# Kernel optimization log

Measured on AMD Instinct MI355X. Metric: run time of the kernel, lower is better.

The kernel has to match this reference:

```python
import jax, jax.numpy as jnp
import numpy as np

N_NODES = 100000
N_EDGES = 3200000
N_GRAPHS = 2048
MOL_DIM = 78
HID = 32
OUT = 128
N_LAYERS = 5
BN_EPS = 1e-5


def setup_inputs() -> dict:
    key = jax.random.key(0)
    ks = jax.random.split(key, 16)
    x = jax.random.normal(ks[0], (N_NODES, MOL_DIM), dtype=jnp.float32)
    edge_index = jax.random.randint(ks[1], (2, N_EDGES), 0, N_NODES, dtype=jnp.int32)
    batch = jnp.sort(jax.random.randint(ks[2], (N_NODES,), 0, N_GRAPHS, dtype=jnp.int32))
    def lin(k, fan_in, shape):
        b = 1.0 / np.sqrt(fan_in)
        return jax.random.uniform(k, shape, jnp.float32, -b, b)
    # layer 0 MLP (78 -> 32 -> 32)
    w1_0 = lin(ks[3], MOL_DIM, (MOL_DIM, HID))
    b1_0 = lin(ks[4], MOL_DIM, (HID,))
    w2_0 = lin(ks[5], HID, (HID, HID))
    b2_0 = lin(ks[6], HID, (HID,))
    # layers 1..4 MLPs (32 -> 32 -> 32), stacked
    w1 = lin(ks[7], HID, (N_LAYERS - 1, HID, HID))
    b1 = lin(ks[8], HID, (N_LAYERS - 1, HID))
    w2 = lin(ks[9], HID, (N_LAYERS - 1, HID, HID))
    b2 = lin(ks[10], HID, (N_LAYERS - 1, HID))
    # BatchNorm affine params per layer
    gamma = jnp.ones((N_LAYERS, HID), jnp.float32)
    beta = jnp.zeros((N_LAYERS, HID), jnp.float32)
    # final fc (32 -> 128)
    fc_w = lin(ks[11], HID, (HID, OUT))
    fc_b = lin(ks[12], HID, (OUT,))
    return {"x": x, "edge_index": edge_index, "batch": batch,
            "w1_0": w1_0, "b1_0": b1_0, "w2_0": w2_0, "b2_0": b2_0,
            "w1": w1, "b1": b1, "w2": w2, "b2": b2,
            "gamma": gamma, "beta": beta, "fc_w": fc_w, "fc_b": fc_b}


def _gin_layer(x, src, dst, W1, B1, W2, B2, g, bt):
    # GIN aggregation: (1+eps)*x + sum_{j in N(i)} x_j, eps = 0
    agg = x + jax.ops.segment_sum(x[src], dst, num_segments=N_NODES)
    h = jnp.maximum(agg @ W1 + B1, 0.0)   # Linear + ReLU
    h = h @ W2 + B2                        # Linear
    h = jnp.maximum(h, 0.0)                # outer act before BN
    mean = jnp.mean(h, axis=0)
    var = jnp.mean(jnp.square(h - mean), axis=0)  # biased (training BN)
    return (h - mean) * jax.lax.rsqrt(var + BN_EPS) * g + bt


def reference(x, edge_index, batch, w1_0, b1_0, w2_0, b2_0,
              w1, b1, w2, b2, gamma, beta, fc_w, fc_b):
    src, dst = edge_index[0], edge_index[1]
    h = _gin_layer(x, src, dst, w1_0, b1_0, w2_0, b2_0, gamma[0], beta[0])
    for i in range(N_LAYERS - 1):
        h = _gin_layer(h, src, dst, w1[i], b1[i], w2[i], b2[i],
                       gamma[i + 1], beta[i + 1])
    pooled = jax.ops.segment_sum(h, batch, num_segments=N_GRAPHS)  # [G, HID]
    out = jnp.maximum(pooled @ fc_w + fc_b, 0.0)  # dropout is identity in eval
    return out
```

## Files before the change

kernel.cpp:

```cpp
#include <hip/hip_runtime.h>
#include <hip/hip_fp16.h>

#define N_NODES 100000
#define N_EDGES 3200000
#define N_GRAPHS 2048
#define MOL 78
#define HID 32
#define OUTD 128
#define BN_EPS 1e-5f

#define NBUCK ((N_NODES + 255) / 256)
#define BCAP2 9216
#define EPB 4096
#define P1_BLOCKS ((N_EDGES + EPB - 1) / EPB)

#define NPH 4
#define CPL_BLOCKS (N_NODES / (8 * NPH))

#define NCOPY 64

__device__ inline unsigned int pkh2(float a, float b) {
    __half2 h = __halves2half2(__float2half_rn(a), __float2half_rn(b));
    return *(unsigned int*)&h;
}
__device__ inline float hlo(unsigned int v) {
    __half2 h = *(__half2*)&v;
    return __low2float(h);
}
__device__ inline float hhi(unsigned int v) {
    __half2 h = *(__half2*)&v;
    return __high2float(h);
}


__global__ __launch_bounds__(256) void part1_kernel(const int* __restrict__ src,
                                                    const int* __restrict__ dst,
                                                    int* __restrict__ gcur,
                                                    int* __restrict__ staging) {
    __shared__ int hist[NBUCK];
    __shared__ int lofs[NBUCK];
    __shared__ int lcur[NBUCK];
    __shared__ int gb[NBUCK];
    __shared__ int pk[EPB];
    __shared__ unsigned short bkt[EPB];
    __shared__ int sc[256];
    const int t = threadIdx.x;
    const int base = blockIdx.x * EPB;
    const int nedge = min(EPB, N_EDGES - base);

    for (int i = t; i < NBUCK; i += 256) hist[i] = 0;
    __syncthreads();
    for (int i = t; i < nedge; i += 256) atomicAdd(&hist[dst[base + i] >> 8], 1);
    __syncthreads();

    int a0 = (2 * t < NBUCK) ? hist[2 * t] : 0;
    int a1 = (2 * t + 1 < NBUCK) ? hist[2 * t + 1] : 0;
    int tot = a0 + a1;
    sc[t] = tot;
    __syncthreads();
    for (int off = 1; off < 256; off <<= 1) {
        int add = (t >= off) ? sc[t - off] : 0;
        __syncthreads();
        sc[t] += add;
        __syncthreads();
    }
    int excl = sc[t] - tot;
    if (2 * t < NBUCK) { lofs[2 * t] = excl; lcur[2 * t] = excl; }
    if (2 * t + 1 < NBUCK) { lofs[2 * t + 1] = excl + a0; lcur[2 * t + 1] = excl + a0; }
    __syncthreads();

    for (int i = t; i < nedge; i += 256) {
        int d = dst[base + i];
        int s = src[base + i];
        int b = d >> 8;
        int p = atomicAdd(&lcur[b], 1);
        pk[p] = (s << 8) | (d & 255);
        bkt[p] = (unsigned short)b;
    }
    __syncthreads();

    for (int b = t; b < NBUCK; b += 256) {
        int c = lcur[b] - lofs[b];
        gb[b] = c ? atomicAdd(&gcur[b], c) : 0;
    }
    __syncthreads();

    for (int i = t; i < nedge; i += 256) {
        int b = bkt[i];
        staging[(size_t)b * BCAP2 + gb[b] + (i - lofs[b])] = pk[i];
    }
}

__global__ void csrbase_kernel(const int* __restrict__ gcur, int* __restrict__ bbase,
                               int* __restrict__ row_start) {
    int t = threadIdx.x;
    int a0 = (2 * t < NBUCK) ? gcur[2 * t] : 0;
    int a1 = (2 * t + 1 < NBUCK) ? gcur[2 * t + 1] : 0;
    int tot = a0 + a1;
    __shared__ int sc[256];
    sc[t] = tot;
    __syncthreads();
    for (int off = 1; off < 256; off <<= 1) {
        int add = (t >= off) ? sc[t - off] : 0;
        __syncthreads();
        sc[t] += add;
        __syncthreads();
    }
    int excl = sc[t] - tot;
    if (2 * t < NBUCK) bbase[2 * t] = excl;
    if (2 * t + 1 < NBUCK) bbase[2 * t + 1] = excl + a0;
    if (t == 0) row_start[N_NODES] = N_EDGES;
}

__global__ __launch_bounds__(256) void part2_kernel(const int* __restrict__ gcur,
                                                    const int* __restrict__ bbase,
                                                    const int* __restrict__ staging,
                                                    int* __restrict__ row_start,
                                                    int* __restrict__ csr,
                                                    float* __restrict__ degf) {
    int b = blockIdx.x, t = threadIdx.x;
    __shared__ int ldeg[256];
    __shared__ int lex[256];
    __shared__ int sc[256];
    ldeg[t] = 0;
    __syncthreads();
    int cnt = gcur[b];
    int base = bbase[b];
    const int* sp = staging + (size_t)b * BCAP2;
    for (int i = t; i < cnt; i += 256) atomicAdd(&ldeg[sp[i] & 255], 1);
    __syncthreads();
    int v = ldeg[t];
    sc[t] = v;
    __syncthreads();
    for (int off = 1; off < 256; off <<= 1) {
        int add = (t >= off) ? sc[t - off] : 0;
        __syncthreads();
        sc[t] += add;
        __syncthreads();
    }
    int excl = sc[t] - v;
    int node = b * 256 + t;
    if (node < N_NODES) {
        row_start[node] = base + excl;
        degf[node] = 1.0f + (float)v;
    }
    lex[t] = base + excl;
    __syncthreads();
    for (int i = t; i < cnt; i += 256) {
        int pk = sp[i];
        int p = atomicAdd(&lex[pk & 255], 1);
        csr[p] = pk >> 8;
    }
}


__global__ void gcnt_kernel(const int* __restrict__ batch, int* __restrict__ cnt) {
    int g = blockIdx.x * blockDim.x + threadIdx.x;
    if (g >= N_GRAPHS) return;
    auto lb = [&](int key) {
        int lo = 0, hi = N_NODES;
        while (lo < hi) {
            int mid = (lo + hi) >> 1;
            if (batch[mid] < key) lo = mid + 1; else hi = mid;
        }
        return lo;
    };
    cnt[g] = lb(g + 1) - lb(g);
}


__global__ __launch_bounds__(256) void proj78_kernel(const float* __restrict__ in,
                                                     const float* __restrict__ W1,
                                                     unsigned int* __restrict__ y) {
    __shared__ float w1s[MOL * HID];
    for (int i = threadIdx.x; i < MOL * HID; i += 256) w1s[i] = W1[i];
    __syncthreads();
    const int node = blockIdx.x * 256 + threadIdx.x;
    if (node >= N_NODES) return;
    const float* row = in + (size_t)node * MOL;
    float acc[HID];
#pragma unroll
    for (int j = 0; j < HID; j++) acc[j] = 0.f;
    const float4* w1v = (const float4*)w1s;
    for (int k = 0; k < MOL; k++) {
        float xv = row[k];
#pragma unroll
        for (int q = 0; q < 8; q++) {
            float4 wv = w1v[k * 8 + q];
            acc[4 * q + 0] = fmaf(xv, wv.x, acc[4 * q + 0]);
            acc[4 * q + 1] = fmaf(xv, wv.y, acc[4 * q + 1]);
            acc[4 * q + 2] = fmaf(xv, wv.z, acc[4 * q + 2]);
            acc[4 * q + 3] = fmaf(xv, wv.w, acc[4 * q + 3]);
        }
    }
    uint4* o = (uint4*)(y + (size_t)node * 16);
#pragma unroll
    for (int g = 0; g < 4; g++) {
        uint4 u;
        u.x = pkh2(acc[8 * g + 0], acc[8 * g + 1]);
        u.y = pkh2(acc[8 * g + 2], acc[8 * g + 3]);
        u.z = pkh2(acc[8 * g + 4], acc[8 * g + 5]);
        u.w = pkh2(acc[8 * g + 6], acc[8 * g + 7]);
        o[g] = u;
    }
}


template <int MODE>
__global__ __launch_bounds__(256) void gma_kernel(
    const unsigned int* __restrict__ y, const int* __restrict__ rs, const int* __restrict__ csr,
    const float* __restrict__ degf, const float* __restrict__ scsh_prev,
    const float* __restrict__ B1, const float* __restrict__ W1, const float* __restrict__ W2,
    const float* __restrict__ B2, __half* __restrict__ out, float* __restrict__ sums,
    const int* __restrict__ batch, float* __restrict__ pooledraw) {
    __shared__ float ldsu[8][NPH][HID];
    __shared__ float ldsv[8][NPH][HID];
    __shared__ float w2T[HID][HID + 1];
    __shared__ float w1T[HID][HID + 1];
    __shared__ float ssum[64];
    const int t = threadIdx.x;
    const int hw = t >> 5;
    const int hl = t & 31;
    const int s = hl >> 2;
    const int q = hl & 3;
    const int c = hl;

    for (int idx = t; idx < HID * HID; idx += 256) {
        int k = idx >> 5, cc = idx & 31;
        w2T[cc][k] = W2[idx];
        if (MODE != 0) w1T[cc][k] = W1[idx];
    }
    if (t < 64) ssum[t] = 0.f;
    __syncthreads();

    float4 p0a, p0b, p1a, p1b;
    if (MODE == 0) {
        p0a = ((const float4*)B1)[2 * q];
        p0b = ((const float4*)B1)[2 * q + 1];
    } else {
        p0a = ((const float4*)scsh_prev)[2 * q];
        p0b = ((const float4*)scsh_prev)[2 * q + 1];
        p1a = ((const float4*)(scsh_prev + HID))[2 * q];
        p1b = ((const float4*)(scsh_prev + HID))[2 * q + 1];
    }

    const int n0 = (blockIdx.x * 8 + hw) * NPH;
    const uint4* rows = (const uint4*)y;

    for (int u = 0; u < NPH; u++) {
        const int n = n0 + u;
        float acc[8];
#pragma unroll
        for (int i = 0; i < 8; i++) acc[i] = 0.f;
        if (s == 0) {
            uint4 w = rows[(size_t)n * 4 + q];
            acc[0] = hlo(w.x); acc[1] = hhi(w.x);
            acc[2] = hlo(w.y); acc[3] = hhi(w.y);
            acc[4] = hlo(w.z); acc[5] = hhi(w.z);
            acc[6] = hlo(w.w); acc[7] = hhi(w.w);
        }
        int e0 = rs[n], e1 = rs[n + 1];
        int k = e0 + s;
        for (; k + 8 < e1; k += 16) {
            uint4 a = rows[(size_t)csr[k] * 4 + q];
            uint4 b = rows[(size_t)csr[k + 8] * 4 + q];
            acc[0] += hlo(a.x) + hlo(b.x);
            acc[1] += hhi(a.x) + hhi(b.x);
            acc[2] += hlo(a.y) + hlo(b.y);
            acc[3] += hhi(a.y) + hhi(b.y);
            acc[4] += hlo(a.z) + hlo(b.z);
            acc[5] += hhi(a.z) + hhi(b.z);
            acc[6] += hlo(a.w) + hlo(b.w);
            acc[7] += hhi(a.w) + hhi(b.w);
        }
        if (k < e1) {
            uint4 a = rows[(size_t)csr[k] * 4 + q];
            acc[0] += hlo(a.x); acc[1] += hhi(a.x);
            acc[2] += hlo(a.y); acc[3] += hhi(a.y);
            acc[4] += hlo(a.z); acc[5] += hhi(a.z);
            acc[6] += hlo(a.w); acc[7] += hhi(a.w);
        }
#pragma unroll
        for (int m = 4; m <= 16; m <<= 1) {
#pragma unroll
            for (int i = 0; i < 8; i++) acc[i] += __shfl_xor(acc[i], m, 32);
        }
        if (s == 0) {
            float o[8];
            if (MODE == 0) {
                o[0] = fmaxf(acc[0] + p0a.x, 0.f); o[1] = fmaxf(acc[1] + p0a.y, 0.f);
                o[2] = fmaxf(acc[2] + p0a.z, 0.f); o[3] = fmaxf(acc[3] + p0a.w, 0.f);
                o[4] = fmaxf(acc[4] + p0b.x, 0.f); o[5] = fmaxf(acc[5] + p0b.y, 0.f);
                o[6] = fmaxf(acc[6] + p0b.z, 0.f); o[7] = fmaxf(acc[7] + p0b.w, 0.f);
            } else {
                float dn = degf[n];
                o[0] = fmaf(acc[0], p0a.x, dn * p1a.x);
                o[1] = fmaf(acc[1], p0a.y, dn * p1a.y);
                o[2] = fmaf(acc[2], p0a.z, dn * p1a.z);
                o[3] = fmaf(acc[3], p0a.w, dn * p1a.w);
                o[4] = fmaf(acc[4], p0b.x, dn * p1b.x);
                o[5] = fmaf(acc[5], p0b.y, dn * p1b.y);
                o[6] = fmaf(acc[6], p0b.z, dn * p1b.z);
                o[7] = fmaf(acc[7], p0b.w, dn * p1b.w);
            }
            float4* d = (float4*)&ldsu[hw][u][q * 8];
            d[0] = make_float4(o[0], o[1], o[2], o[3]);
            d[1] = make_float4(o[4], o[5], o[6], o[7]);
        }
    }

    const float b2c = B2[c];
    float sl = 0.f, sq = 0.f;

    if (MODE == 0) {
        float h[NPH];
#pragma unroll
        for (int u = 0; u < NPH; u++) h[u] = b2c;
#pragma unroll
        for (int qq = 0; qq < 8; qq++) {
            float wa = w2T[c][4 * qq + 0], wb = w2T[c][4 * qq + 1];
            float wc2 = w2T[c][4 * qq + 2], wd = w2T[c][4 * qq + 3];
#pragma unroll
            for (int u = 0; u < NPH; u++) {
                float4 vv = ((const float4*)&ldsu[hw][u][0])[qq];
                h[u] = fmaf(vv.x, wa, h[u]);
                h[u] = fmaf(vv.y, wb, h[u]);
                h[u] = fmaf(vv.z, wc2, h[u]);
                h[u] = fmaf(vv.w, wd, h[u]);
            }
        }
#pragma unroll
        for (int u = 0; u < NPH; u++) {
            float hv = fmaxf(h[u], 0.f);
            out[(size_t)(n0 + u) * 32 + c] = __float2half_rn(hv);
            sl += hv;
            sq += hv * hv;
        }
    } else {
        const float b1c = B1[c];
        float tv[NPH];
#pragma unroll
        for (int u = 0; u < NPH; u++) tv[u] = b1c;
#pragma unroll
        for (int qq = 0; qq < 8; qq++) {
            float wa = w1T[c][4 * qq + 0], wb = w1T[c][4 * qq + 1];
            float wc1 = w1T[c][4 * qq + 2], wd = w1T[c][4 * qq + 3];
#pragma unroll
            for (int u = 0; u < NPH; u++) {
                float4 uu = ((const float4*)&ldsu[hw][u][0])[qq];
                tv[u] = fmaf(uu.x, wa, tv[u]);
                tv[u] = fmaf(uu.y, wb, tv[u]);
                tv[u] = fmaf(uu.z, wc1, tv[u]);
                tv[u] = fmaf(uu.w, wd, tv[u]);
            }
        }
#pragma unroll
        for (int u = 0; u < NPH; u++) ldsv[hw][u][c] = fmaxf(tv[u], 0.f);
        float h[NPH];
#pragma unroll
        for (int u = 0; u < NPH; u++) h[u] = b2c;
#pragma unroll
        for (int qq = 0; qq < 8; qq++) {
            float wa = w2T[c][4 * qq + 0], wb = w2T[c][4 * qq + 1];
            float wc2 = w2T[c][4 * qq + 2], wd = w2T[c][4 * qq + 3];
#pragma unroll
            for (int u = 0; u < NPH; u++) {
                float4 vv = ((const float4*)&ldsv[hw][u][0])[qq];
                h[u] = fmaf(vv.x, wa, h[u]);
                h[u] = fmaf(vv.y, wb, h[u]);
                h[u] = fmaf(vv.z, wc2, h[u]);
                h[u] = fmaf(vv.w, wd, h[u]);
            }
        }
#pragma unroll
        for (int u = 0; u < NPH; u++) {
            float hv = fmaxf(h[u], 0.f);
            if (MODE == 2) {
                atomicAdd(&pooledraw[batch[n0 + u] * HID + c], hv);
            } else {
                out[(size_t)(n0 + u) * 32 + c] = __float2half_rn(hv);
            }
            sl += hv;
            sq += hv * hv;
        }
    }

    atomicAdd(&ssum[c], sl);
    atomicAdd(&ssum[32 + c], sq);
    __syncthreads();
    if (t < 64) atomicAdd(&sums[(blockIdx.x & (NCOPY - 1)) * 64 + t], ssum[t]);
}


__global__ void bnfin_kernel(const float* __restrict__ sums, const float* __restrict__ g,
                             const float* __restrict__ bt, float* __restrict__ scsh) {
    __shared__ float red[64];
    int t = threadIdx.x;
    if (t < 64) {
        float acc = 0.f;
#pragma unroll 8
        for (int k = 0; k < NCOPY; k++) acc += sums[k * 64 + t];
        red[t] = acc;
    }
    __syncthreads();
    if (t < HID) {
        float m = red[t] * (1.0f / N_NODES);
        float var = red[HID + t] * (1.0f / N_NODES) - m * m;
        var = fmaxf(var, 0.f);
        float sc = g[t] * rsqrtf(var + BN_EPS);
        scsh[t] = sc;
        scsh[HID + t] = bt[t] - m * sc;
    }
}


__global__ void fc_kernel(const float* __restrict__ praw, const int* __restrict__ cnt,
                          const float* __restrict__ scsh4, const float* __restrict__ fcw,
                          const float* __restrict__ fcb, float* __restrict__ out) {
    __shared__ float w[HID * OUTD];
    __shared__ float aff[2 * HID];
    for (int i = threadIdx.x; i < HID * OUTD; i += 256) w[i] = fcw[i];
    if (threadIdx.x < 2 * HID) aff[threadIdx.x] = scsh4[threadIdx.x];
    __syncthreads();
    int idx = blockIdx.x * 256 + threadIdx.x;
    if (idx >= N_GRAPHS * OUTD) return;
    int g = idx >> 7;
    int o = idx & 127;
    float cg = (float)cnt[g];
    float acc = fcb[o];
#pragma unroll
    for (int k = 0; k < HID; k++) {
        float paff = fmaf(praw[g * HID + k], aff[k], cg * aff[HID + k]);
        acc = fmaf(paff, w[k * OUTD + o], acc);
    }
    out[idx] = fmaxf(acc, 0.f);
}


extern "C" void kernel_launch(void* const* d_in, const int* in_sizes, int n_in,
                              void* d_out, int out_size, void* d_ws, size_t ws_size,
                              hipStream_t stream) {
    const float* x = (const float*)d_in[0];
    const int* ei = (const int*)d_in[1];
    const int* batch = (const int*)d_in[2];
    const float* w1_0 = (const float*)d_in[3];
    const float* b1_0 = (const float*)d_in[4];
    const float* w2_0 = (const float*)d_in[5];
    const float* b2_0 = (const float*)d_in[6];
    const float* w1 = (const float*)d_in[7];
    const float* b1 = (const float*)d_in[8];
    const float* w2 = (const float*)d_in[9];
    const float* b2 = (const float*)d_in[10];
    const float* gamma = (const float*)d_in[11];
    const float* beta = (const float*)d_in[12];
    const float* fc_w = (const float*)d_in[13];
    const float* fc_b = (const float*)d_in[14];
    float* out = (float*)d_out;

    const int* e_src = ei;
    const int* e_dst = ei + N_EDGES;

    char* ws = (char*)d_ws;
    size_t off = 0;
    auto alloc = [&](size_t n) {
        void* p = ws + off;
        off += (n + 255) & ~(size_t)255;
        return p;
    };
    int* row_start = (int*)alloc((size_t)(N_NODES + 1) * 4);
    int* csr = (int*)alloc((size_t)N_EDGES * 4);
    int* bbase = (int*)alloc((size_t)NBUCK * 4);
    int* staging = (int*)alloc((size_t)NBUCK * BCAP2 * 4);
    unsigned int* hA = (unsigned int*)alloc((size_t)N_NODES * 16 * 4);
    unsigned int* hB = (unsigned int*)alloc((size_t)N_NODES * 16 * 4);
    float* degf = (float*)alloc((size_t)N_NODES * 4);
    float* scsh = (float*)alloc(5 * 2 * HID * 4);
    int* cnt = (int*)alloc((size_t)N_GRAPHS * 4);
    size_t zero_base = off;
    int* gcur = (int*)alloc((size_t)NBUCK * 4);
    float* bnsums = (float*)alloc((size_t)5 * NCOPY * 64 * 4);
    float* pooled = (float*)alloc((size_t)N_GRAPHS * HID * 4);
    size_t zero_len = off - zero_base;

    hipMemsetAsync(ws + zero_base, 0, zero_len, stream);

    part1_kernel<<<P1_BLOCKS, 256, 0, stream>>>(e_src, e_dst, gcur, staging);
    csrbase_kernel<<<1, 256, 0, stream>>>(gcur, bbase, row_start);
    part2_kernel<<<NBUCK, 256, 0, stream>>>(gcur, bbase, staging, row_start, csr, degf);
    gcnt_kernel<<<(N_GRAPHS + 255) / 256, 256, 0, stream>>>(batch, cnt);

    const int nodeBlocks = (N_NODES + 255) / 256;

    proj78_kernel<<<nodeBlocks, 256, 0, stream>>>(x, w1_0, hA);
    gma_kernel<0><<<CPL_BLOCKS, 256, 0, stream>>>(
        hA, row_start, csr, nullptr, nullptr, b1_0, nullptr, w2_0, b2_0, (__half*)hB, bnsums,
        nullptr, nullptr);
    bnfin_kernel<<<1, 64, 0, stream>>>(bnsums, gamma, beta, scsh);

    unsigned int* cur = hB;
    unsigned int* nxt = hA;
    for (int l = 1; l < 5; l++) {
        int i = l - 1;
        if (l < 4) {
            gma_kernel<1><<<CPL_BLOCKS, 256, 0, stream>>>(
                cur, row_start, csr, degf, scsh + (l - 1) * 2 * HID, b1 + (size_t)i * HID,
                w1 + (size_t)i * HID * HID, w2 + (size_t)i * HID * HID, b2 + (size_t)i * HID,
                (__half*)nxt, bnsums + (size_t)l * NCOPY * 64, nullptr, nullptr);
            unsigned int* tmp = cur; cur = nxt; nxt = tmp;
        } else {
            gma_kernel<2><<<CPL_BLOCKS, 256, 0, stream>>>(
                cur, row_start, csr, degf, scsh + (l - 1) * 2 * HID, b1 + (size_t)i * HID,
                w1 + (size_t)i * HID * HID, w2 + (size_t)i * HID * HID, b2 + (size_t)i * HID,
                nullptr, bnsums + (size_t)l * NCOPY * 64, batch, pooled);
        }
        bnfin_kernel<<<1, 64, 0, stream>>>(bnsums + (size_t)l * NCOPY * 64, gamma + l * HID,
                                           beta + l * HID, scsh + l * 2 * HID);
    }

    fc_kernel<<<(N_GRAPHS * OUTD + 255) / 256, 256, 0, stream>>>(
        pooled, cnt, scsh + 4 * 2 * HID, fc_w, fc_b, out);
}
```

Before: 410.9 us.

## Split fused gather-MLP kernel into separate aggregation and MLP kernels

The fused gather+MLP kernel is split in two. A standalone aggregation kernel assigns one node per 32-lane group and writes fp32 neighbor sums to a new buffer, and a separate MLP kernel reads those sums to apply BN scale/shift, the two linear layers and the statistics. The aim is more parallelism and latency hiding in the gather, which previously walked 4 nodes serially per half-wave. The cost is an extra fp32 round trip through global memory (12.8 MB written and read per layer) and five more kernel launches.

```diff
diff --git a/kernel.cpp b/kernel.cpp
--- a/kernel.cpp
+++ b/kernel.cpp
@@ -206,13 +206,68 @@
 }
 
 
+__global__ __launch_bounds__(256) void agg_kernel(const unsigned int* __restrict__ y,
+                                                  const int* __restrict__ rs,
+                                                  const int* __restrict__ csr,
+                                                  float* __restrict__ agg) {
+    int gt = blockIdx.x * blockDim.x + threadIdx.x;
+    int node = gt >> 5;
+    if (node >= N_NODES) return;
+    int hl = threadIdx.x & 31;
+    int s = hl >> 2;
+    int q = hl & 3;
+    const uint4* rows = (const uint4*)y;
+    float acc[8];
+#pragma unroll
+    for (int i = 0; i < 8; i++) acc[i] = 0.f;
+    if (s == 0) {
+        uint4 u = rows[(size_t)node * 4 + q];
+        acc[0] = hlo(u.x); acc[1] = hhi(u.x);
+        acc[2] = hlo(u.y); acc[3] = hhi(u.y);
+        acc[4] = hlo(u.z); acc[5] = hhi(u.z);
+        acc[6] = hlo(u.w); acc[7] = hhi(u.w);
+    }
+    int e0 = rs[node], e1 = rs[node + 1];
+    int k = e0 + s;
+    for (; k + 8 < e1; k += 16) {
+        uint4 a = rows[(size_t)csr[k] * 4 + q];
+        uint4 b = rows[(size_t)csr[k + 8] * 4 + q];
+        acc[0] += hlo(a.x) + hlo(b.x);
+        acc[1] += hhi(a.x) + hhi(b.x);
+        acc[2] += hlo(a.y) + hlo(b.y);
+        acc[3] += hhi(a.y) + hhi(b.y);
+        acc[4] += hlo(a.z) + hlo(b.z);
+        acc[5] += hhi(a.z) + hhi(b.z);
+        acc[6] += hlo(a.w) + hlo(b.w);
+        acc[7] += hhi(a.w) + hhi(b.w);
+    }
+    if (k < e1) {
+        uint4 a = rows[(size_t)csr[k] * 4 + q];
+        acc[0] += hlo(a.x); acc[1] += hhi(a.x);
+        acc[2] += hlo(a.y); acc[3] += hhi(a.y);
+        acc[4] += hlo(a.z); acc[5] += hhi(a.z);
+        acc[6] += hlo(a.w); acc[7] += hhi(a.w);
+    }
+#pragma unroll
+    for (int m = 4; m <= 16; m <<= 1) {
+#pragma unroll
+        for (int i = 0; i < 8; i++) acc[i] += __shfl_xor(acc[i], m, 32);
+    }
+    if (s == 0) {
+        float4* o = (float4*)(agg + (size_t)node * HID + q * 8);
+        o[0] = make_float4(acc[0], acc[1], acc[2], acc[3]);
+        o[1] = make_float4(acc[4], acc[5], acc[6], acc[7]);
+    }
+}
+
+
 template <int MODE>
-__global__ __launch_bounds__(256) void gma_kernel(
-    const unsigned int* __restrict__ y, const int* __restrict__ rs, const int* __restrict__ csr,
-    const float* __restrict__ degf, const float* __restrict__ scsh_prev,
-    const float* __restrict__ B1, const float* __restrict__ W1, const float* __restrict__ W2,
-    const float* __restrict__ B2, __half* __restrict__ out, float* __restrict__ sums,
-    const int* __restrict__ batch, float* __restrict__ pooledraw) {
+__global__ __launch_bounds__(256) void mlp_kernel(
+    const float* __restrict__ aggb, const float* __restrict__ degf,
+    const float* __restrict__ scsh_prev, const float* __restrict__ B1,
+    const float* __restrict__ W1, const float* __restrict__ W2, const float* __restrict__ B2,
+    __half* __restrict__ out, float* __restrict__ sums, const int* __restrict__ batch,
+    float* __restrict__ pooledraw) {
     __shared__ float ldsu[8][NPH][HID];
     __shared__ float ldsv[8][NPH][HID];
     __shared__ float w2T[HID][HID + 1];
@@ -220,10 +275,7 @@
     __shared__ float ssum[64];
     const int t = threadIdx.x;
     const int hw = t >> 5;
-    const int hl = t & 31;
-    const int s = hl >> 2;
-    const int q = hl & 3;
-    const int c = hl;
+    const int c = t & 31;
 
     for (int idx = t; idx < HID * HID; idx += 256) {
         int k = idx >> 5, cc = idx & 31;
@@ -233,86 +285,15 @@
     if (t < 64) ssum[t] = 0.f;
     __syncthreads();
 
-    float4 p0a, p0b, p1a, p1b;
-    if (MODE == 0) {
-        p0a = ((const float4*)B1)[2 * q];
-        p0b = ((const float4*)B1)[2 * q + 1];
-    } else {
-        p0a = ((const float4*)scsh_prev)[2 * q];
-        p0b = ((const float4*)scsh_prev)[2 * q + 1];
-        p1a = ((const float4*)(scsh_prev + HID))[2 * q];
-        p1b = ((const float4*)(scsh_prev + HID))[2 * q + 1];
-    }
-
     const int n0 = (blockIdx.x * 8 + hw) * NPH;
-    const uint4* rows = (const uint4*)y;
-
-    for (int u = 0; u < NPH; u++) {
-        const int n = n0 + u;
-        float acc[8];
-#pragma unroll
-        for (int i = 0; i < 8; i++) acc[i] = 0.f;
-        if (s == 0) {
-            uint4 w = rows[(size_t)n * 4 + q];
-            acc[0] = hlo(w.x); acc[1] = hhi(w.x);
-            acc[2] = hlo(w.y); acc[3] = hhi(w.y);
-            acc[4] = hlo(w.z); acc[5] = hhi(w.z);
-            acc[6] = hlo(w.w); acc[7] = hhi(w.w);
-        }
-        int e0 = rs[n], e1 = rs[n + 1];
-        int k = e0 + s;
-        for (; k + 8 < e1; k += 16) {
-            uint4 a = rows[(size_t)csr[k] * 4 + q];
-            uint4 b = rows[(size_t)csr[k + 8] * 4 + q];
-            acc[0] += hlo(a.x) + hlo(b.x);
-            acc[1] += hhi(a.x) + hhi(b.x);
-            acc[2] += hlo(a.y) + hlo(b.y);
-            acc[3] += hhi(a.y) + hhi(b.y);
-            acc[4] += hlo(a.z) + hlo(b.z);
-            acc[5] += hhi(a.z) + hhi(b.z);
-            acc[6] += hlo(a.w) + hlo(b.w);
-            acc[7] += hhi(a.w) + hhi(b.w);
-        }
-        if (k < e1) {
-            uint4 a = rows[(size_t)csr[k] * 4 + q];
-            acc[0] += hlo(a.x); acc[1] += hhi(a.x);
-            acc[2] += hlo(a.y); acc[3] += hhi(a.y);
-            acc[4] += hlo(a.z); acc[5] += hhi(a.z);
-            acc[6] += hlo(a.w); acc[7] += hhi(a.w);
-        }
-#pragma unroll
-        for (int m = 4; m <= 16; m <<= 1) {
-#pragma unroll
-            for (int i = 0; i < 8; i++) acc[i] += __shfl_xor(acc[i], m, 32);
-        }
-        if (s == 0) {
-            float o[8];
-            if (MODE == 0) {
-                o[0] = fmaxf(acc[0] + p0a.x, 0.f); o[1] = fmaxf(acc[1] + p0a.y, 0.f);
-                o[2] = fmaxf(acc[2] + p0a.z, 0.f); o[3] = fmaxf(acc[3] + p0a.w, 0.f);
-                o[4] = fmaxf(acc[4] + p0b.x, 0.f); o[5] = fmaxf(acc[5] + p0b.y, 0.f);
-                o[6] = fmaxf(acc[6] + p0b.z, 0.f); o[7] = fmaxf(acc[7] + p0b.w, 0.f);
-            } else {
-                float dn = degf[n];
-                o[0] = fmaf(acc[0], p0a.x, dn * p1a.x);
-                o[1] = fmaf(acc[1], p0a.y, dn * p1a.y);
-                o[2] = fmaf(acc[2], p0a.z, dn * p1a.z);
-                o[3] = fmaf(acc[3], p0a.w, dn * p1a.w);
-                o[4] = fmaf(acc[4], p0b.x, dn * p1b.x);
-                o[5] = fmaf(acc[5], p0b.y, dn * p1b.y);
-                o[6] = fmaf(acc[6], p0b.z, dn * p1b.z);
-                o[7] = fmaf(acc[7], p0b.w, dn * p1b.w);
-            }
-            float4* d = (float4*)&ldsu[hw][u][q * 8];
-            d[0] = make_float4(o[0], o[1], o[2], o[3]);
-            d[1] = make_float4(o[4], o[5], o[6], o[7]);
-        }
-    }
-
     const float b2c = B2[c];
     float sl = 0.f, sq = 0.f;
 
     if (MODE == 0) {
+        const float b1c = B1[c];
+#pragma unroll
+        for (int u = 0; u < NPH; u++)
+            ldsu[hw][u][c] = fmaxf(aggb[(size_t)(n0 + u) * HID + c] + b1c, 0.f);
         float h[NPH];
 #pragma unroll
         for (int u = 0; u < NPH; u++) h[u] = b2c;
@@ -337,7 +318,13 @@
             sq += hv * hv;
         }
     } else {
+        const float scv = scsh_prev[c], shv = scsh_prev[HID + c];
         const float b1c = B1[c];
+#pragma unroll
+        for (int u = 0; u < NPH; u++) {
+            int n = n0 + u;
+            ldsu[hw][u][c] = fmaf(aggb[(size_t)n * HID + c], scv, degf[n] * shv);
+        }
         float tv[NPH];
 #pragma unroll
         for (int u = 0; u < NPH; u++) tv[u] = b1c;
@@ -473,6 +460,7 @@
     int* staging = (int*)alloc((size_t)NBUCK * BCAP2 * 4);
     unsigned int* hA = (unsigned int*)alloc((size_t)N_NODES * 16 * 4);
     unsigned int* hB = (unsigned int*)alloc((size_t)N_NODES * 16 * 4);
+    float* aggb = (float*)alloc((size_t)N_NODES * HID * 4);
     float* degf = (float*)alloc((size_t)N_NODES * 4);
     float* scsh = (float*)alloc(5 * 2 * HID * 4);
     int* cnt = (int*)alloc((size_t)N_GRAPHS * 4);
@@ -490,26 +478,28 @@
     gcnt_kernel<<<(N_GRAPHS + 255) / 256, 256, 0, stream>>>(batch, cnt);
 
     const int nodeBlocks = (N_NODES + 255) / 256;
+    const int aggBlocks = (N_NODES * 32 + 255) / 256;
 
     proj78_kernel<<<nodeBlocks, 256, 0, stream>>>(x, w1_0, hA);
-    gma_kernel<0><<<CPL_BLOCKS, 256, 0, stream>>>(
-        hA, row_start, csr, nullptr, nullptr, b1_0, nullptr, w2_0, b2_0, (__half*)hB, bnsums,
-        nullptr, nullptr);
+    agg_kernel<<<aggBlocks, 256, 0, stream>>>(hA, row_start, csr, aggb);
+    mlp_kernel<0><<<CPL_BLOCKS, 256, 0, stream>>>(aggb, nullptr, nullptr, b1_0, nullptr, w2_0,
+                                                  b2_0, (__half*)hB, bnsums, nullptr, nullptr);
     bnfin_kernel<<<1, 64, 0, stream>>>(bnsums, gamma, beta, scsh);
 
     unsigned int* cur = hB;
     unsigned int* nxt = hA;
     for (int l = 1; l < 5; l++) {
         int i = l - 1;
+        agg_kernel<<<aggBlocks, 256, 0, stream>>>(cur, row_start, csr, aggb);
         if (l < 4) {
-            gma_kernel<1><<<CPL_BLOCKS, 256, 0, stream>>>(
-                cur, row_start, csr, degf, scsh + (l - 1) * 2 * HID, b1 + (size_t)i * HID,
+            mlp_kernel<1><<<CPL_BLOCKS, 256, 0, stream>>>(
+                aggb, degf, scsh + (l - 1) * 2 * HID, b1 + (size_t)i * HID,
                 w1 + (size_t)i * HID * HID, w2 + (size_t)i * HID * HID, b2 + (size_t)i * HID,
                 (__half*)nxt, bnsums + (size_t)l * NCOPY * 64, nullptr, nullptr);
             unsigned int* tmp = cur; cur = nxt; nxt = tmp;
         } else {
-            gma_kernel<2><<<CPL_BLOCKS, 256, 0, stream>>>(
-                cur, row_start, csr, degf, scsh + (l - 1) * 2 * HID, b1 + (size_t)i * HID,
+            mlp_kernel<2><<<CPL_BLOCKS, 256, 0, stream>>>(
+                aggb, degf, scsh + (l - 1) * 2 * HID, b1 + (size_t)i * HID,
                 w1 + (size_t)i * HID * HID, w2 + (size_t)i * HID * HID, b2 + (size_t)i * HID,
                 nullptr, bnsums + (size_t)l * NCOPY * 64, batch, pooled);
         }
```

Measured after the change: 431.8 us. 5.1% more time.
